# Kernel tuning notes

Measured on AMD Instinct MI355X. Metric: run time of the kernel, lower is better.

Reference implementation:

```python
import math
import jax, jax.numpy as jnp
import numpy as np

RES = [16, 32, 64, 128, 256, 512, 1024, 2048]  # base=16, finest=2048, 8 levels, growth=2
FD = 2            # feature_dim per grid level
LPE_N = 128
NF = 4            # lpe_n_freq
D0 = 8            # lpe_d0
LPE_OUT = D0 + 4 * NF  # 24
HID = 64
T = 4             # num_textures
EPS = 1e-6


def _gather_bilerp(grid, u, v, scale, imax, stride):
    """Bilinear gather from a flattened 2D grid. Returns (feat[B,C], lu[B,1], lv[B,1])."""
    fu = u * scale
    fv = v * scale
    i0 = jnp.clip(jnp.floor(fu).astype(jnp.int32), 0, imax)
    j0 = jnp.clip(jnp.floor(fv).astype(jnp.int32), 0, imax)
    lu = (fu - i0.astype(fu.dtype))[:, None]
    lv = (fv - j0.astype(fv.dtype))[:, None]
    idx00 = i0 + j0 * stride
    f00 = grid[idx00]
    f10 = grid[idx00 + 1]
    f01 = grid[idx00 + stride]
    f11 = grid[idx00 + 1 + stride]
    f0 = f00 * (1.0 - lu) + f10 * lu
    f1 = f01 * (1.0 - lu) + f11 * lu
    return f0 * (1.0 - lv) + f1 * lv, lu, lv


def setup_inputs() -> dict:
    key = jax.random.key(0)
    ks = jax.random.split(key, 24)
    B = 1048576
    inp = {"coords": jax.random.uniform(ks[0], (B, 2), jnp.float32)}
    for i, r in enumerate(RES):
        inp[f"grid{i}"] = jax.random.uniform(ks[1 + i], (r * r, FD), jnp.float32, -1e-4, 1e-4)
    inp["lpe_grid"] = jax.random.uniform(ks[9], ((LPE_N + 1) ** 2, LPE_OUT), jnp.float32, -1e-4, 1e-4)
    in_dim = FD + LPE_OUT  # 26
    inp["w0"] = jax.random.normal(ks[10], (in_dim, HID), jnp.float32) / math.sqrt(in_dim)
    inp["b0"] = jnp.zeros((HID,), jnp.float32)
    inp["w1"] = jax.random.normal(ks[11], (HID, HID), jnp.float32) / math.sqrt(HID)
    inp["b1"] = jnp.zeros((HID,), jnp.float32)
    inp["w2"] = jax.random.normal(ks[12], (HID, T), jnp.float32) / math.sqrt(HID)
    inp["b2"] = jnp.zeros((T,), jnp.float32)
    return inp


def _forward(coords, grids, lpe_grid, w0, b0, w1, b1, w2, b2):
    c = jnp.clip(coords, 0.0, 1.0 - EPS)
    u = c[:, 0]
    v = c[:, 1]
    # Multi-resolution feature grids, residual-fused (sum over levels)
    enc = jnp.zeros((coords.shape[0], FD), jnp.float32)
    for r, g in zip(RES, grids):
        f, _, _ = _gather_bilerp(g, u, v, float(r - 1), r - 2, r)
        enc = enc + f
    # Local positional encoding on (N+1)^2 grid
    coeff, lu, lv = _gather_bilerp(lpe_grid, u, v, float(LPE_N), LPE_N - 1, LPE_N + 1)
    freqs = (2.0 ** jnp.arange(NF, dtype=jnp.float32)) * (2.0 * math.pi)  # [NF]
    uu = lu * freqs[None, :]
    vv = lv * freqs[None, :]
    pe = jnp.concatenate([jnp.cos(uu), jnp.sin(uu), jnp.cos(vv), jnp.sin(vv)], axis=1)  # [B,4*NF]
    base = coeff[:, :D0]
    gate = coeff[:, D0:D0 + 4 * NF]
    lpe_out = jnp.concatenate([base, gate * pe], axis=1)  # [B,LPE_OUT]
    feat = jnp.concatenate([enc, lpe_out], axis=1)  # [B,26]
    h = jax.nn.relu(feat @ w0 + b0)
    h = jax.nn.relu(h @ w1 + b1)
    return jax.nn.sigmoid(h @ w2 + b2)  # [B,T]


def reference(coords, grid0, grid1, grid2, grid3, grid4, grid5, grid6, grid7,
              lpe_grid, w0, b0, w1, b1, w2, b2):
    grids = (grid0, grid1, grid2, grid3, grid4, grid5, grid6, grid7)
    return _forward(coords, grids, lpe_grid, w0, b0, w1, b1, w2, b2)
```

## Files before the change

### kernel.cpp

```cpp
#include <hip/hip_runtime.h>
#include <math.h>

typedef short bf16x8 __attribute__((ext_vector_type(8)));
typedef float f32x16 __attribute__((ext_vector_type(16)));
typedef float f32x4 __attribute__((ext_vector_type(4)));
typedef unsigned u32x4 __attribute__((ext_vector_type(4)));

#define NF 4
#define D0 8
#define LPE_OUT 24
#define NBUCKET 512
#define NROWS   512

#define PART_OFF   17408ULL
#define TOT_OFF    1065984ULL
#define LPE_OFF    1068544ULL
#define SCOORD_OFF 1867776ULL
#define PERM_OFF   10256384ULL
#define G6B_OFF    14450688ULL
#define G7B_OFF    18644992ULL
#define WS_NEED    35422208ULL

__device__ __forceinline__ unsigned f2bf(float x) {
    unsigned u = __float_as_uint(x);
    u = u + 0x7fffu + ((u >> 16) & 1u);
    return u >> 16;
}
__device__ __forceinline__ unsigned pkbf(float a, float b) {
    return f2bf(a) | (f2bf(b) << 16);
}
__device__ __forceinline__ float bflo(unsigned u) { return __uint_as_float(u << 16); }
__device__ __forceinline__ float bfhi(unsigned u) { return __uint_as_float(u & 0xffff0000u); }
__device__ __forceinline__ bf16x8 mkfrag(unsigned w0, unsigned w1, unsigned w2, unsigned w3) {
    u32x4 u = { w0, w1, w2, w3 };
    return __builtin_bit_cast(bf16x8, u);
}

__device__ void prep_body(const float* __restrict__ w0, const float* __restrict__ b0,
                          const float* __restrict__ w1, const float* __restrict__ b1,
                          const float* __restrict__ w2, float* __restrict__ ws, int t)
{
    unsigned short* a0 = (unsigned short*)ws;
    unsigned short* a1 = a0 + 2048;
    unsigned short* a2 = a1 + 4096;
    float* b0c = (float*)(a2 + 2048);
    float* b1c = b0c + 64;

    for (int e = t; e < 2048; e += 256) {
        int tile = e >> 9, lane = (e >> 3) & 63, j = e & 7;
        int m = tile >> 1, ks = tile & 1;
        int row = m * 32 + (lane & 31);
        int k = ks * 16 + (lane >> 5) * 8 + j;
        float v = (k < 26) ? w0[k * 64 + row] : 0.f;
        a0[e] = (unsigned short)f2bf(v);
    }
    for (int e = t; e < 4096; e += 256) {
        int tile = e >> 9, lane = (e >> 3) & 63, j = e & 7;
        int m = tile >> 2, ks = tile & 3;
        int row = m * 32 + (lane & 31);
        int k = ks * 16 + (lane >> 5) * 8 + j;
        a1[e] = (unsigned short)f2bf(w1[k * 64 + row]);
    }
    for (int e = t; e < 2048; e += 256) {
        int ks = e >> 9, lane = (e >> 3) & 63, j = e & 7;
        int row = lane & 31;
        int k = ks * 16 + (lane >> 5) * 8 + j;
        float v = (row < 4) ? w2[k * 4 + row] : 0.f;
        a2[e] = (unsigned short)f2bf(v);
    }
    if (t < 64) {
        int m = t >> 5, q5 = (t >> 4) & 1, r = t & 15;
        int row = (r & 3) + 8 * (r >> 2) + 4 * q5;
        b0c[(m * 2 + q5) * 16 + r] = b0[m * 32 + row];
        b1c[(m * 2 + q5) * 16 + r] = b1[m * 32 + row];
    }
}

__global__ void prep_kernel(const float* __restrict__ w0, const float* __restrict__ b0,
                            const float* __restrict__ w1, const float* __restrict__ b1,
                            const float* __restrict__ w2, float* __restrict__ ws)
{
    prep_body(w0, b0, w1, b1, w2, ws, threadIdx.x);
}

__device__ __forceinline__ int bucket_of(float cx, float cy) {
    float u = fminf(fmaxf(cx, 0.f), 1.f - 1e-6f);
    float v = fminf(fmaxf(cy, 0.f), 1.f - 1e-6f);
    return (int)(v * 32.f) * 16 + (int)(u * 16.f);
}

__global__ __launch_bounds__(256)
void fused_pre(const float2* __restrict__ g6, const float2* __restrict__ g7,
               const float4* __restrict__ lpe4, const float2* __restrict__ coords,
               unsigned* __restrict__ part, unsigned* __restrict__ totals,
               const float* __restrict__ w0, const float* __restrict__ b0,
               const float* __restrict__ w1, const float* __restrict__ b1,
               const float* __restrict__ w2, float* __restrict__ ws, char* __restrict__ wsb)
{
    int b = blockIdx.x, t = threadIdx.x;
    if (b < 16384) {
        int cell = b * 256 + t;
        float2 f = g7[cell];
        ((unsigned*)(wsb + G7B_OFF))[cell] = pkbf(f.x, f.y);
        return;
    }
    if (b < 20480) {
        int cell = (b - 16384) * 256 + t;
        float2 f = g6[cell];
        ((unsigned*)(wsb + G6B_OFF))[cell] = pkbf(f.x, f.y);
        return;
    }
    if (b < 20676) {
        int i = (b - 20480) * 256 + t;
        if (i < 49923) {
            float4 a = lpe4[i * 2], c = lpe4[i * 2 + 1];
            u32x4 o = { pkbf(a.x, a.y), pkbf(a.z, a.w), pkbf(c.x, c.y), pkbf(c.z, c.w) };
            ((u32x4*)(wsb + LPE_OFF))[i] = o;
        }
        return;
    }
    if (b < 21188) {
        int hb = b - 20676;
        __shared__ unsigned h[NBUCKET];
        h[t] = 0; h[t + 256] = 0;
        __syncthreads();
        for (int k = 0; k < 8; ++k) {
            float2 c = coords[hb * 2048 + k * 256 + t];
            atomicAdd(&h[bucket_of(c.x, c.y)], 1u);
        }
        __syncthreads();
        unsigned v0 = h[t], v1 = h[t + 256];
        part[hb * NBUCKET + t] = v0;
        part[hb * NBUCKET + 256 + t] = v1;
        if (v0) atomicAdd(&totals[t], v0);
        if (v1) atomicAdd(&totals[t + 256], v1);
        return;
    }
    prep_body(w0, b0, w1, b1, w2, ws, t);
}

__global__ __launch_bounds__(256)
void sort_offsets(unsigned* __restrict__ part, const unsigned* __restrict__ totals)
{
    int bucket = blockIdx.x, t = threadIdx.x;
    __shared__ unsigned red[256];
    unsigned s0 = (t < bucket) ? totals[t] : 0u;
    if (t + 256 < bucket) s0 += totals[t + 256];
    red[t] = s0;
    __syncthreads();
    for (int off = 128; off > 0; off >>= 1) {
        if (t < off) red[t] += red[t + off];
        __syncthreads();
    }
    unsigned start = red[0];
    __syncthreads();

    unsigned l0 = part[(2 * t) * NBUCKET + bucket];
    unsigned l1 = part[(2 * t + 1) * NBUCKET + bucket];
    unsigned s = l0 + l1;
    __shared__ unsigned sc[256];
    sc[t] = s;
    __syncthreads();
    for (int off = 1; off < 256; off <<= 1) {
        unsigned v = (t >= off) ? sc[t - off] : 0u;
        __syncthreads();
        sc[t] += v;
        __syncthreads();
    }
    unsigned base = start + sc[t] - s;
    part[(2 * t) * NBUCKET + bucket] = base;
    part[(2 * t + 1) * NBUCKET + bucket] = base + l0;
}

__global__ __launch_bounds__(256)
void sort_scatter(const float2* __restrict__ coords, const unsigned* __restrict__ offs,
                  float2* __restrict__ scoord, unsigned* __restrict__ perm)
{
    __shared__ unsigned cnt[NBUCKET];
    __shared__ unsigned base[NBUCKET];
    int t = threadIdx.x, hb = blockIdx.x;
    cnt[t] = 0; cnt[t + 256] = 0;
    base[t] = offs[hb * NBUCKET + t];
    base[t + 256] = offs[hb * NBUCKET + 256 + t];
    __syncthreads();
    for (int k = 0; k < 8; ++k) {
        int i = hb * 2048 + k * 256 + t;
        float2 c = coords[i];
        int bb = bucket_of(c.x, c.y);
        unsigned r = atomicAdd(&cnt[bb], 1u);
        unsigned slot = base[bb] + r;
        scoord[slot] = c;
        perm[slot] = (unsigned)i;
    }
}

__device__ __forceinline__ void mlp_pair(const unsigned (&B0)[2][2][4],
                                         const float* __restrict__ ws,
                                         const float* __restrict__ b2,
                                         int lane, int q5, f32x16 (&acc2)[2])
{
    const bf16x8* A0 = (const bf16x8*)ws;
    const bf16x8* A1 = (const bf16x8*)((const char*)ws + 4096);
    const bf16x8* A2 = (const bf16x8*)((const char*)ws + 12288);
    const float4* b0c = (const float4*)((const char*)ws + 16384);
    const float4* b1c = (const float4*)((const char*)ws + 16640);

    unsigned B1[4][2][4];
#pragma unroll
    for (int m = 0; m < 2; ++m) {
        f32x16 acc[2];
#pragma unroll
        for (int cc = 0; cc < 4; ++cc) {
            float4 bq = b0c[(m * 2 + q5) * 4 + cc];
#pragma unroll
            for (int n = 0; n < 2; ++n) {
                acc[n][4 * cc + 0] = bq.x;
                acc[n][4 * cc + 1] = bq.y;
                acc[n][4 * cc + 2] = bq.z;
                acc[n][4 * cc + 3] = bq.w;
            }
        }
#pragma unroll
        for (int ks = 0; ks < 2; ++ks) {
            bf16x8 af = A0[(m * 2 + ks) * 64 + lane];
#pragma unroll
            for (int n = 0; n < 2; ++n)
                acc[n] = __builtin_amdgcn_mfma_f32_32x32x16_bf16(
                    af, mkfrag(B0[ks][n][0], B0[ks][n][1], B0[ks][n][2], B0[ks][n][3]),
                    acc[n], 0, 0, 0);
        }
#pragma unroll
        for (int t = 0; t < 2; ++t) {
#pragma unroll
            for (int n = 0; n < 2; ++n)
#pragma unroll
                for (int c = 0; c < 2; ++c) {
                    int r0 = 2 * c + 8 * t;
                    int r1 = 2 * c + 8 * t + 4;
                    unsigned P0 = pkbf(fmaxf(acc[n][r0], 0.f), fmaxf(acc[n][r0 + 1], 0.f));
                    unsigned P1 = pkbf(fmaxf(acc[n][r1], 0.f), fmaxf(acc[n][r1 + 1], 0.f));
                    auto r = __builtin_amdgcn_permlane32_swap(P1, P0, false, false);
                    B1[2 * m + t][n][c] = r[1];
                    B1[2 * m + t][n][2 + c] = r[0];
                }
        }
    }

    unsigned B2[4][2][4];
#pragma unroll
    for (int m = 0; m < 2; ++m) {
        f32x16 acc[2];
#pragma unroll
        for (int cc = 0; cc < 4; ++cc) {
            float4 bq = b1c[(m * 2 + q5) * 4 + cc];
#pragma unroll
            for (int n = 0; n < 2; ++n) {
                acc[n][4 * cc + 0] = bq.x;
                acc[n][4 * cc + 1] = bq.y;
                acc[n][4 * cc + 2] = bq.z;
                acc[n][4 * cc + 3] = bq.w;
            }
        }
#pragma unroll
        for (int ks = 0; ks < 4; ++ks) {
            bf16x8 af = A1[(m * 4 + ks) * 64 + lane];
#pragma unroll
            for (int n = 0; n < 2; ++n)
                acc[n] = __builtin_amdgcn_mfma_f32_32x32x16_bf16(
                    af, mkfrag(B1[ks][n][0], B1[ks][n][1], B1[ks][n][2], B1[ks][n][3]),
                    acc[n], 0, 0, 0);
        }
#pragma unroll
        for (int t = 0; t < 2; ++t) {
#pragma unroll
            for (int n = 0; n < 2; ++n)
#pragma unroll
                for (int c = 0; c < 2; ++c) {
                    int r0 = 2 * c + 8 * t;
                    int r1 = 2 * c + 8 * t + 4;
                    unsigned P0 = pkbf(fmaxf(acc[n][r0], 0.f), fmaxf(acc[n][r0 + 1], 0.f));
                    unsigned P1 = pkbf(fmaxf(acc[n][r1], 0.f), fmaxf(acc[n][r1 + 1], 0.f));
                    auto r = __builtin_amdgcn_permlane32_swap(P1, P0, false, false);
                    B2[2 * m + t][n][c] = r[1];
                    B2[2 * m + t][n][2 + c] = r[0];
                }
        }
    }

#pragma unroll
    for (int n = 0; n < 2; ++n)
#pragma unroll
        for (int r = 0; r < 16; ++r) acc2[n][r] = (r < 4) ? b2[r] : 0.f;
#pragma unroll
    for (int ks = 0; ks < 4; ++ks) {
        bf16x8 af = A2[ks * 64 + lane];
#pragma unroll
        for (int n = 0; n < 2; ++n)
            acc2[n] = __builtin_amdgcn_mfma_f32_32x32x16_bf16(
                af, mkfrag(B2[ks][n][0], B2[ks][n][1], B2[ks][n][2], B2[ks][n][3]),
                acc2[n], 0, 0, 0);
    }
}

__global__ __launch_bounds__(256, 4)
void colornet_sorted(const float2* __restrict__ pts,
                     const unsigned* __restrict__ perm,
                     const float2* __restrict__ g0, const float2* __restrict__ g1,
                     const float2* __restrict__ g2, const float2* __restrict__ g3,
                     const float2* __restrict__ g4, const float2* __restrict__ g5,
                     const float* __restrict__ ws,
                     const float* __restrict__ b2,
                     f32x4* __restrict__ out)
{
    const int lane = threadIdx.x & 63;
    const int wave = threadIdx.x >> 6;
    const int q5 = lane >> 5;
    int bid = blockIdx.x;
    int cpx = gridDim.x >> 3;
    bid = (bid & 7) * cpx + (bid >> 3);
    const int base_pt = bid * 256 + wave * 64;
    const char* wsb = (const char*)ws;

    float2 c = pts[base_pt + lane];
    float uA = fminf(fmaxf(c.x, 0.f), 1.f - 1e-6f);
    float vA = fminf(fmaxf(c.y, 0.f), 1.f - 1e-6f);

    float e0A = 0.f, e1A = 0.f;

#define ADDR(IDX, R) int gx##IDX; float lu##IDX, lv##IDX; \
    { float fu_ = uA * (float)((R) - 1), fv_ = vA * (float)((R) - 1); \
      int i0_ = (int)floorf(fu_), j0_ = (int)floorf(fv_); \
      i0_ = i0_ < 0 ? 0 : (i0_ > (R) - 2 ? (R) - 2 : i0_); \
      j0_ = j0_ < 0 ? 0 : (j0_ > (R) - 2 ? (R) - 2 : j0_); \
      lu##IDX = fu_ - (float)i0_; lv##IDX = fv_ - (float)j0_; \
      gx##IDX = i0_ + j0_ * (R); }
    ADDR(7, 2048) ADDR(6, 1024) ADDR(5, 512) ADDR(4, 256)
    ADDR(3, 128)  ADDR(2, 64)   ADDR(1, 32)  ADDR(0, 16)

    const unsigned* G7 = (const unsigned*)(wsb + G7B_OFF);
    const unsigned* G6 = (const unsigned*)(wsb + G6B_OFF);
    unsigned t7_0 = G7[gx7], t7_1 = G7[gx7 + 1], t7_2 = G7[gx7 + 2048], t7_3 = G7[gx7 + 2049];
    unsigned t6_0 = G6[gx6], t6_1 = G6[gx6 + 1], t6_2 = G6[gx6 + 1024], t6_3 = G6[gx6 + 1025];

#define LOADF(IDX, R, G) \
    float2 f##IDX##_0 = (G)[gx##IDX],       f##IDX##_1 = (G)[gx##IDX + 1], \
           f##IDX##_2 = (G)[gx##IDX + (R)], f##IDX##_3 = (G)[gx##IDX + (R) + 1];
    LOADF(5, 512, g5) LOADF(4, 256, g4) LOADF(3, 128, g3)
    LOADF(2, 64,  g2) LOADF(1, 32,  g1) LOADF(0, 16,  g0)

    float lu_pe, lv_pe;
    int lc;
    {
        float fu = uA * 128.f, fv = vA * 128.f;
        int i0 = (int)floorf(fu);
        int j0 = (int)floorf(fv);
        i0 = i0 < 0 ? 0 : (i0 > 127 ? 127 : i0);
        j0 = j0 < 0 ? 0 : (j0 > 127 ? 127 : j0);
        lu_pe = fu - (float)i0;
        lv_pe = fv - (float)j0;
        lc = (i0 + j0 * 129) * 3;
    }
    const u32x4* LP = (const u32x4*)(wsb + LPE_OFF);
    u32x4 L00a = LP[lc],       L00b = LP[lc + 1],   L00c = LP[lc + 2];
    u32x4 L10a = LP[lc + 3],   L10b = LP[lc + 4],   L10c = LP[lc + 5];
    u32x4 L01a = LP[lc + 387], L01b = LP[lc + 388], L01c = LP[lc + 389];
    u32x4 L11a = LP[lc + 390], L11b = LP[lc + 391], L11c = LP[lc + 392];

    float peA[16];
#pragma unroll
    for (int kf = 0; kf < NF; ++kf) {
        float au = lu_pe * (float)(1 << kf);
        float av = lv_pe * (float)(1 << kf);
        float fu_ = __builtin_amdgcn_fractf(au);
        float fv_ = __builtin_amdgcn_fractf(av);
        peA[kf]          = __builtin_amdgcn_cosf(fu_);
        peA[NF + kf]     = __builtin_amdgcn_sinf(fu_);
        peA[2 * NF + kf] = __builtin_amdgcn_cosf(fv_);
        peA[3 * NF + kf] = __builtin_amdgcn_sinf(fv_);
    }

#define WGT(IDX) float omu##IDX = 1.f - lu##IDX, omv##IDX = 1.f - lv##IDX; \
    float w00##IDX = omu##IDX * omv##IDX, w10##IDX = lu##IDX * omv##IDX, \
          w01##IDX = omu##IDX * lv##IDX,  w11##IDX = lu##IDX * lv##IDX;
    { WGT(7)
      e0A += bflo(t7_0) * w007 + bflo(t7_1) * w107 + bflo(t7_2) * w017 + bflo(t7_3) * w117;
      e1A += bfhi(t7_0) * w007 + bfhi(t7_1) * w107 + bfhi(t7_2) * w017 + bfhi(t7_3) * w117; }
    { WGT(6)
      e0A += bflo(t6_0) * w006 + bflo(t6_1) * w106 + bflo(t6_2) * w016 + bflo(t6_3) * w116;
      e1A += bfhi(t6_0) * w006 + bfhi(t6_1) * w106 + bfhi(t6_2) * w016 + bfhi(t6_3) * w116; }
#define SUMF(IDX) { WGT(IDX) \
      e0A += f##IDX##_0.x * w00##IDX + f##IDX##_1.x * w10##IDX + f##IDX##_2.x * w01##IDX + f##IDX##_3.x * w11##IDX; \
      e1A += f##IDX##_0.y * w00##IDX + f##IDX##_1.y * w10##IDX + f##IDX##_2.y * w01##IDX + f##IDX##_3.y * w11##IDX; }
    SUMF(5) SUMF(4) SUMF(3) SUMF(2) SUMF(1) SUMF(0)

    float coeffA[LPE_OUT];
    {
        float omu = 1.f - lu_pe, omv = 1.f - lv_pe;
        float q00 = omu * omv, q10 = lu_pe * omv, q01 = omu * lv_pe, q11 = lu_pe * lv_pe;
#define LPW(W, A, B, C, Dd) \
        coeffA[2*(W)]   = bflo(A)*q00 + bflo(B)*q10 + bflo(C)*q01 + bflo(Dd)*q11; \
        coeffA[2*(W)+1] = bfhi(A)*q00 + bfhi(B)*q10 + bfhi(C)*q01 + bfhi(Dd)*q11;
        LPW(0,  L00a[0], L10a[0], L01a[0], L11a[0])
        LPW(1,  L00a[1], L10a[1], L01a[1], L11a[1])
        LPW(2,  L00a[2], L10a[2], L01a[2], L11a[2])
        LPW(3,  L00a[3], L10a[3], L01a[3], L11a[3])
        LPW(4,  L00b[0], L10b[0], L01b[0], L11b[0])
        LPW(5,  L00b[1], L10b[1], L01b[1], L11b[1])
        LPW(6,  L00b[2], L10b[2], L01b[2], L11b[2])
        LPW(7,  L00b[3], L10b[3], L01b[3], L11b[3])
        LPW(8,  L00c[0], L10c[0], L01c[0], L11c[0])
        LPW(9,  L00c[1], L10c[1], L01c[1], L11c[1])
        LPW(10, L00c[2], L10c[2], L01c[2], L11c[2])
        LPW(11, L00c[3], L10c[3], L01c[3], L11c[3])
#undef LPW
    }

    unsigned fdA[16];
    {
        float feat[32];
        feat[0] = e0A; feat[1] = e1A;
#pragma unroll
        for (int q = 0; q < D0; ++q) feat[2 + q] = coeffA[q];
#pragma unroll
        for (int q = 0; q < 4 * NF; ++q) feat[2 + D0 + q] = coeffA[D0 + q] * peA[q];
#pragma unroll
        for (int q = 26; q < 32; ++q) feat[q] = 0.f;
#pragma unroll
        for (int i = 0; i < 16; ++i) fdA[i] = pkbf(feat[2 * i], feat[2 * i + 1]);
    }

    unsigned B0a[2][2][4];
#pragma unroll
    for (int ks = 0; ks < 2; ++ks)
#pragma unroll
        for (int j2 = 0; j2 < 4; ++j2) {
            unsigned a = fdA[8 * ks + j2];
            unsigned b = fdA[8 * ks + 4 + j2];
            auto r = __builtin_amdgcn_permlane32_swap(b, a, false, false);
            B0a[ks][1][j2] = r[0];
            B0a[ks][0][j2] = r[1];
        }

    f32x16 acc2[2];
    mlp_pair(B0a, ws, b2, lane, q5, acc2);

    if (lane < 32) {
#pragma unroll
        for (int n = 0; n < 2; ++n) {
            f32x4 o;
            o[0] = 1.f / (1.f + __expf(-acc2[n][0]));
            o[1] = 1.f / (1.f + __expf(-acc2[n][1]));
            o[2] = 1.f / (1.f + __expf(-acc2[n][2]));
            o[3] = 1.f / (1.f + __expf(-acc2[n][3]));
            int oi = (int)perm[base_pt + 32 * n + lane];
            __builtin_nontemporal_store(o, out + oi);
        }
    }
}

template<int R>
__device__ __forceinline__ void gather_level(const float* __restrict__ g,
                                             float u, float v,
                                             float& e0, float& e1) {
    const float scale = (float)(R - 1);
    float fu = u * scale, fv = v * scale;
    int i0 = (int)floorf(fu);
    int j0 = (int)floorf(fv);
    i0 = i0 < 0 ? 0 : (i0 > R - 2 ? R - 2 : i0);
    j0 = j0 < 0 ? 0 : (j0 > R - 2 ? R - 2 : j0);
    float lu = fu - (float)i0;
    float lv = fv - (float)j0;
    const float2* gg = (const float2*)g;
    int base = i0 + j0 * R;
    float2 f00 = gg[base];
    float2 f10 = gg[base + 1];
    float2 f01 = gg[base + R];
    float2 f11 = gg[base + R + 1];
    float omu = 1.f - lu, omv = 1.f - lv;
    float w00 = omu * omv, w10 = lu * omv, w01 = omu * lv, w11 = lu * lv;
    e0 += f00.x * w00 + f10.x * w10 + f01.x * w01 + f11.x * w11;
    e1 += f00.y * w00 + f10.y * w10 + f01.y * w01 + f11.y * w11;
}

__global__ __launch_bounds__(256, 4)
void colornet_fp32(const float* __restrict__ coords,
                   const float* __restrict__ g0, const float* __restrict__ g1,
                   const float* __restrict__ g2, const float* __restrict__ g3,
                   const float* __restrict__ g4, const float* __restrict__ g5,
                   const float* __restrict__ g6, const float* __restrict__ g7,
                   const float* __restrict__ lpe,
                   const float* __restrict__ ws,
                   const float* __restrict__ b2,
                   f32x4* __restrict__ out)
{
    const int lane = threadIdx.x & 63;
    const int wave = threadIdx.x >> 6;
    const int q5 = lane >> 5;
    const int base_pt = blockIdx.x * 256 + wave * 64;
    const int point = base_pt + lane;

    const float* cp = coords + 2 * point;
    float cx = __builtin_nontemporal_load(cp);
    float cy = __builtin_nontemporal_load(cp + 1);
    float uA = fminf(fmaxf(cx, 0.f), 1.f - 1e-6f);
    float vA = fminf(fmaxf(cy, 0.f), 1.f - 1e-6f);

    float e0 = 0.f, e1 = 0.f;
    gather_level<16>(g0, uA, vA, e0, e1);
    gather_level<32>(g1, uA, vA, e0, e1);
    gather_level<64>(g2, uA, vA, e0, e1);
    gather_level<128>(g3, uA, vA, e0, e1);
    gather_level<256>(g4, uA, vA, e0, e1);
    gather_level<512>(g5, uA, vA, e0, e1);
    gather_level<1024>(g6, uA, vA, e0, e1);
    gather_level<2048>(g7, uA, vA, e0, e1);

    float coeff[LPE_OUT];
    float lu_pe, lv_pe;
    {
        float fu = uA * 128.f, fv = vA * 128.f;
        int i0 = (int)floorf(fu);
        int j0 = (int)floorf(fv);
        i0 = i0 < 0 ? 0 : (i0 > 127 ? 127 : i0);
        j0 = j0 < 0 ? 0 : (j0 > 127 ? 127 : j0);
        lu_pe = fu - (float)i0;
        lv_pe = fv - (float)j0;
        int base = (i0 + j0 * 129) * LPE_OUT;
        const float4* p00 = (const float4*)(lpe + base);
        const float4* p10 = (const float4*)(lpe + base + LPE_OUT);
        const float4* p01 = (const float4*)(lpe + base + 129 * LPE_OUT);
        const float4* p11 = (const float4*)(lpe + base + 130 * LPE_OUT);
        float omu = 1.f - lu_pe, omv = 1.f - lv_pe;
        float w00 = omu * omv, w10 = lu_pe * omv, w01 = omu * lv_pe, w11 = lu_pe * lv_pe;
#pragma unroll
        for (int q = 0; q < 6; ++q) {
            float4 a = p00[q], bq = p10[q], cq = p01[q], dq = p11[q];
            coeff[4 * q + 0] = a.x * w00 + bq.x * w10 + cq.x * w01 + dq.x * w11;
            coeff[4 * q + 1] = a.y * w00 + bq.y * w10 + cq.y * w01 + dq.y * w11;
            coeff[4 * q + 2] = a.z * w00 + bq.z * w10 + cq.z * w01 + dq.z * w11;
            coeff[4 * q + 3] = a.w * w00 + bq.w * w10 + cq.w * w01 + dq.w * w11;
        }
    }

    float pe[16];
#pragma unroll
    for (int kf = 0; kf < NF; ++kf) {
        const float fr = 6.28318530717958647692f * (float)(1 << kf);
        float au = lu_pe * fr;
        float av = lv_pe * fr;
        pe[kf]          = __cosf(au);
        pe[NF + kf]     = __sinf(au);
        pe[2 * NF + kf] = __cosf(av);
        pe[3 * NF + kf] = __sinf(av);
    }

    float feat[32];
    feat[0] = e0; feat[1] = e1;
#pragma unroll
    for (int q = 0; q < D0; ++q) feat[2 + q] = coeff[q];
#pragma unroll
    for (int q = 0; q < 4 * NF; ++q) feat[2 + D0 + q] = coeff[D0 + q] * pe[q];
#pragma unroll
    for (int q = 26; q < 32; ++q) feat[q] = 0.f;

    unsigned fd[16];
#pragma unroll
    for (int i = 0; i < 16; ++i) fd[i] = pkbf(feat[2 * i], feat[2 * i + 1]);

    unsigned B0[2][2][4];
#pragma unroll
    for (int ks = 0; ks < 2; ++ks)
#pragma unroll
        for (int j2 = 0; j2 < 4; ++j2) {
            unsigned a = fd[8 * ks + j2];
            unsigned b = fd[8 * ks + 4 + j2];
            auto r = __builtin_amdgcn_permlane32_swap(b, a, false, false);
            B0[ks][1][j2] = r[0];
            B0[ks][0][j2] = r[1];
        }

    f32x16 acc2[2];
    mlp_pair(B0, ws, b2, lane, q5, acc2);
    if (lane < 32) {
#pragma unroll
        for (int n = 0; n < 2; ++n) {
            f32x4 o;
            o[0] = 1.f / (1.f + __expf(-acc2[n][0]));
            o[1] = 1.f / (1.f + __expf(-acc2[n][1]));
            o[2] = 1.f / (1.f + __expf(-acc2[n][2]));
            o[3] = 1.f / (1.f + __expf(-acc2[n][3]));
            __builtin_nontemporal_store(o, out + (base_pt + 32 * n + lane));
        }
    }
}

extern "C" void kernel_launch(void* const* d_in, const int* in_sizes, int n_in,
                              void* d_out, int out_size, void* d_ws, size_t ws_size,
                              hipStream_t stream) {
    const float* coords = (const float*)d_in[0];
    const float* g0 = (const float*)d_in[1];
    const float* g1 = (const float*)d_in[2];
    const float* g2 = (const float*)d_in[3];
    const float* g3 = (const float*)d_in[4];
    const float* g4 = (const float*)d_in[5];
    const float* g5 = (const float*)d_in[6];
    const float* g6 = (const float*)d_in[7];
    const float* g7 = (const float*)d_in[8];
    const float* lpe = (const float*)d_in[9];
    const float* w0 = (const float*)d_in[10];
    const float* b0 = (const float*)d_in[11];
    const float* w1 = (const float*)d_in[12];
    const float* b1 = (const float*)d_in[13];
    const float* w2 = (const float*)d_in[14];
    const float* b2 = (const float*)d_in[15];
    f32x4* out = (f32x4*)d_out;

    int B = in_sizes[0] / 2;
    char* wsb = (char*)d_ws;

    if (ws_size >= WS_NEED && B == 1048576) {
        unsigned* part   = (unsigned*)(wsb + PART_OFF);
        unsigned* totals = (unsigned*)(wsb + TOT_OFF);
        float2*   scoord = (float2*)(wsb + SCOORD_OFF);
        unsigned* perm   = (unsigned*)(wsb + PERM_OFF);
        const float2* c2 = (const float2*)coords;

        (void)hipMemsetAsync(totals, 0, NBUCKET * sizeof(unsigned), stream);
        fused_pre<<<21189, 256, 0, stream>>>((const float2*)g6, (const float2*)g7,
                                             (const float4*)lpe, c2, part, totals,
                                             w0, b0, w1, b1, w2, (float*)d_ws, wsb);
        sort_offsets<<<NBUCKET, 256, 0, stream>>>(part, totals);
        sort_scatter<<<NROWS, 256, 0, stream>>>(c2, part, scoord, perm);

        colornet_sorted<<<4096, 256, 0, stream>>>(scoord, perm,
                                                  (const float2*)g0, (const float2*)g1,
                                                  (const float2*)g2, (const float2*)g3,
                                                  (const float2*)g4, (const float2*)g5,
                                                  (const float*)d_ws, b2, out);
    } else {
        prep_kernel<<<1, 256, 0, stream>>>(w0, b0, w1, b1, w2, (float*)d_ws);
        colornet_fp32<<<B / 256, 256, 0, stream>>>(coords, g0, g1, g2, g3, g4, g5, g6, g7,
                                                   lpe, (const float*)d_ws, b2, out);
    }
}
```

Baseline: 122.0 us.

## Read LPE grid directly in fp32 and vectorize bilinear math with float2

Removes the pre-pass that converted the LPE coefficient grid to bf16 in workspace, so the main kernel now gathers the 24 fp32 coefficients per corner straight from the input as float4 loads. This drops 196 blocks from the fused preprocessing launch. Accumulations switch to 2-wide float vectors, which can lower to packed FMA instructions, and bf16 packing now goes through the HIP intrinsic. The cost is twice the gather bytes per LPE corner in the main kernel, on a grid of about 4.8 MB that likely stays cache-resident.

```diff
diff --git a/kernel.cpp b/kernel.cpp
--- a/kernel.cpp
+++ b/kernel.cpp
@@ -1,9 +1,11 @@
 #include <hip/hip_runtime.h>
+#include <hip/hip_bf16.h>
 #include <math.h>
 
 typedef short bf16x8 __attribute__((ext_vector_type(8)));
 typedef float f32x16 __attribute__((ext_vector_type(16)));
 typedef float f32x4 __attribute__((ext_vector_type(4)));
+typedef float f32x2 __attribute__((ext_vector_type(2)));
 typedef unsigned u32x4 __attribute__((ext_vector_type(4)));
 
 #define NF 4
@@ -14,7 +16,6 @@
 
 #define PART_OFF   17408ULL
 #define TOT_OFF    1065984ULL
-#define LPE_OFF    1068544ULL
 #define SCOORD_OFF 1867776ULL
 #define PERM_OFF   10256384ULL
 #define G6B_OFF    14450688ULL
@@ -27,10 +28,16 @@
     return u >> 16;
 }
 __device__ __forceinline__ unsigned pkbf(float a, float b) {
-    return f2bf(a) | (f2bf(b) << 16);
+    __hip_bfloat16 ha = __float2bfloat16(a);
+    __hip_bfloat16 hb = __float2bfloat16(b);
+    unsigned short ua, ub;
+    __builtin_memcpy(&ua, &ha, 2);
+    __builtin_memcpy(&ub, &hb, 2);
+    return (unsigned)ua | ((unsigned)ub << 16);
 }
 __device__ __forceinline__ float bflo(unsigned u) { return __uint_as_float(u << 16); }
 __device__ __forceinline__ float bfhi(unsigned u) { return __uint_as_float(u & 0xffff0000u); }
+__device__ __forceinline__ f32x2 bf2(unsigned u) { f32x2 r = { bflo(u), bfhi(u) }; return r; }
 __device__ __forceinline__ bf16x8 mkfrag(unsigned w0, unsigned w1, unsigned w2, unsigned w3) {
     u32x4 u = { w0, w1, w2, w3 };
     return __builtin_bit_cast(bf16x8, u);
@@ -91,7 +98,7 @@
 
 __global__ __launch_bounds__(256)
 void fused_pre(const float2* __restrict__ g6, const float2* __restrict__ g7,
-               const float4* __restrict__ lpe4, const float2* __restrict__ coords,
+               const float2* __restrict__ coords,
                unsigned* __restrict__ part, unsigned* __restrict__ totals,
                const float* __restrict__ w0, const float* __restrict__ b0,
                const float* __restrict__ w1, const float* __restrict__ b1,
@@ -110,17 +117,8 @@
         ((unsigned*)(wsb + G6B_OFF))[cell] = pkbf(f.x, f.y);
         return;
     }
-    if (b < 20676) {
-        int i = (b - 20480) * 256 + t;
-        if (i < 49923) {
-            float4 a = lpe4[i * 2], c = lpe4[i * 2 + 1];
-            u32x4 o = { pkbf(a.x, a.y), pkbf(a.z, a.w), pkbf(c.x, c.y), pkbf(c.z, c.w) };
-            ((u32x4*)(wsb + LPE_OFF))[i] = o;
-        }
-        return;
-    }
-    if (b < 21188) {
-        int hb = b - 20676;
+    if (b < 20992) {
+        int hb = b - 20480;
         __shared__ unsigned h[NBUCKET];
         h[t] = 0; h[t + 256] = 0;
         __syncthreads();
@@ -305,9 +303,10 @@
 __global__ __launch_bounds__(256, 4)
 void colornet_sorted(const float2* __restrict__ pts,
                      const unsigned* __restrict__ perm,
-                     const float2* __restrict__ g0, const float2* __restrict__ g1,
-                     const float2* __restrict__ g2, const float2* __restrict__ g3,
-                     const float2* __restrict__ g4, const float2* __restrict__ g5,
+                     const f32x2* __restrict__ g0, const f32x2* __restrict__ g1,
+                     const f32x2* __restrict__ g2, const f32x2* __restrict__ g3,
+                     const f32x2* __restrict__ g4, const f32x2* __restrict__ g5,
+                     const float* __restrict__ lpe,
                      const float* __restrict__ ws,
                      const float* __restrict__ b2,
                      f32x4* __restrict__ out)
@@ -324,8 +323,6 @@
     float2 c = pts[base_pt + lane];
     float uA = fminf(fmaxf(c.x, 0.f), 1.f - 1e-6f);
     float vA = fminf(fmaxf(c.y, 0.f), 1.f - 1e-6f);
-
-    float e0A = 0.f, e1A = 0.f;
 
 #define ADDR(IDX, R) int gx##IDX; float lu##IDX, lv##IDX; \
     { float fu_ = uA * (float)((R) - 1), fv_ = vA * (float)((R) - 1); \
@@ -343,13 +340,13 @@
     unsigned t6_0 = G6[gx6], t6_1 = G6[gx6 + 1], t6_2 = G6[gx6 + 1024], t6_3 = G6[gx6 + 1025];
 
 #define LOADF(IDX, R, G) \
-    float2 f##IDX##_0 = (G)[gx##IDX],       f##IDX##_1 = (G)[gx##IDX + 1], \
-           f##IDX##_2 = (G)[gx##IDX + (R)], f##IDX##_3 = (G)[gx##IDX + (R) + 1];
+    f32x2 f##IDX##_0 = (G)[gx##IDX],       f##IDX##_1 = (G)[gx##IDX + 1], \
+          f##IDX##_2 = (G)[gx##IDX + (R)], f##IDX##_3 = (G)[gx##IDX + (R) + 1];
     LOADF(5, 512, g5) LOADF(4, 256, g4) LOADF(3, 128, g3)
     LOADF(2, 64,  g2) LOADF(1, 32,  g1) LOADF(0, 16,  g0)
 
     float lu_pe, lv_pe;
-    int lc;
+    const float4 *p00, *p10, *p01, *p11;
     {
         float fu = uA * 128.f, fv = vA * 128.f;
         int i0 = (int)floorf(fu);
@@ -358,76 +355,65 @@
         j0 = j0 < 0 ? 0 : (j0 > 127 ? 127 : j0);
         lu_pe = fu - (float)i0;
         lv_pe = fv - (float)j0;
-        lc = (i0 + j0 * 129) * 3;
-    }
-    const u32x4* LP = (const u32x4*)(wsb + LPE_OFF);
-    u32x4 L00a = LP[lc],       L00b = LP[lc + 1],   L00c = LP[lc + 2];
-    u32x4 L10a = LP[lc + 3],   L10b = LP[lc + 4],   L10c = LP[lc + 5];
-    u32x4 L01a = LP[lc + 387], L01b = LP[lc + 388], L01c = LP[lc + 389];
-    u32x4 L11a = LP[lc + 390], L11b = LP[lc + 391], L11c = LP[lc + 392];
-
-    float peA[16];
+        int base = (i0 + j0 * 129) * LPE_OUT;
+        p00 = (const float4*)(lpe + base);
+        p10 = (const float4*)(lpe + base + LPE_OUT);
+        p01 = (const float4*)(lpe + base + 129 * LPE_OUT);
+        p11 = (const float4*)(lpe + base + 130 * LPE_OUT);
+    }
+
+    float pe[16];
 #pragma unroll
     for (int kf = 0; kf < NF; ++kf) {
         float au = lu_pe * (float)(1 << kf);
         float av = lv_pe * (float)(1 << kf);
         float fu_ = __builtin_amdgcn_fractf(au);
         float fv_ = __builtin_amdgcn_fractf(av);
-        peA[kf]          = __builtin_amdgcn_cosf(fu_);
-        peA[NF + kf]     = __builtin_amdgcn_sinf(fu_);
-        peA[2 * NF + kf] = __builtin_amdgcn_cosf(fv_);
-        peA[3 * NF + kf] = __builtin_amdgcn_sinf(fv_);
-    }
-
+        pe[kf]          = __builtin_amdgcn_cosf(fu_);
+        pe[NF + kf]     = __builtin_amdgcn_sinf(fu_);
+        pe[2 * NF + kf] = __builtin_amdgcn_cosf(fv_);
+        pe[3 * NF + kf] = __builtin_amdgcn_sinf(fv_);
+    }
+
+    f32x2 eA = { 0.f, 0.f };
 #define WGT(IDX) float omu##IDX = 1.f - lu##IDX, omv##IDX = 1.f - lv##IDX; \
     float w00##IDX = omu##IDX * omv##IDX, w10##IDX = lu##IDX * omv##IDX, \
           w01##IDX = omu##IDX * lv##IDX,  w11##IDX = lu##IDX * lv##IDX;
     { WGT(7)
-      e0A += bflo(t7_0) * w007 + bflo(t7_1) * w107 + bflo(t7_2) * w017 + bflo(t7_3) * w117;
-      e1A += bfhi(t7_0) * w007 + bfhi(t7_1) * w107 + bfhi(t7_2) * w017 + bfhi(t7_3) * w117; }
+      eA += bf2(t7_0) * w007 + bf2(t7_1) * w107 + bf2(t7_2) * w017 + bf2(t7_3) * w117; }
     { WGT(6)
-      e0A += bflo(t6_0) * w006 + bflo(t6_1) * w106 + bflo(t6_2) * w016 + bflo(t6_3) * w116;
-      e1A += bfhi(t6_0) * w006 + bfhi(t6_1) * w106 + bfhi(t6_2) * w016 + bfhi(t6_3) * w116; }
+      eA += bf2(t6_0) * w006 + bf2(t6_1) * w106 + bf2(t6_2) * w016 + bf2(t6_3) * w116; }
 #define SUMF(IDX) { WGT(IDX) \
-      e0A += f##IDX##_0.x * w00##IDX + f##IDX##_1.x * w10##IDX + f##IDX##_2.x * w01##IDX + f##IDX##_3.x * w11##IDX; \
-      e1A += f##IDX##_0.y * w00##IDX + f##IDX##_1.y * w10##IDX + f##IDX##_2.y * w01##IDX + f##IDX##_3.y * w11##IDX; }
+      eA += f##IDX##_0 * w00##IDX + f##IDX##_1 * w10##IDX + f##IDX##_2 * w01##IDX + f##IDX##_3 * w11##IDX; }
     SUMF(5) SUMF(4) SUMF(3) SUMF(2) SUMF(1) SUMF(0)
 
-    float coeffA[LPE_OUT];
+    f32x2 cf[12];
     {
         float omu = 1.f - lu_pe, omv = 1.f - lv_pe;
         float q00 = omu * omv, q10 = lu_pe * omv, q01 = omu * lv_pe, q11 = lu_pe * lv_pe;
-#define LPW(W, A, B, C, Dd) \
-        coeffA[2*(W)]   = bflo(A)*q00 + bflo(B)*q10 + bflo(C)*q01 + bflo(Dd)*q11; \
-        coeffA[2*(W)+1] = bfhi(A)*q00 + bfhi(B)*q10 + bfhi(C)*q01 + bfhi(Dd)*q11;
-        LPW(0,  L00a[0], L10a[0], L01a[0], L11a[0])
-        LPW(1,  L00a[1], L10a[1], L01a[1], L11a[1])
-        LPW(2,  L00a[2], L10a[2], L01a[2], L11a[2])
-        LPW(3,  L00a[3], L10a[3], L01a[3], L11a[3])
-        LPW(4,  L00b[0], L10b[0], L01b[0], L11b[0])
-        LPW(5,  L00b[1], L10b[1], L01b[1], L11b[1])
-        LPW(6,  L00b[2], L10b[2], L01b[2], L11b[2])
-        LPW(7,  L00b[3], L10b[3], L01b[3], L11b[3])
-        LPW(8,  L00c[0], L10c[0], L01c[0], L11c[0])
-        LPW(9,  L00c[1], L10c[1], L01c[1], L11c[1])
-        LPW(10, L00c[2], L10c[2], L01c[2], L11c[2])
-        LPW(11, L00c[3], L10c[3], L01c[3], L11c[3])
-#undef LPW
+#pragma unroll
+        for (int q = 0; q < 6; ++q) {
+            float4 a = p00[q], bq = p10[q], cq = p01[q], dq = p11[q];
+            f32x2 alo = { a.x, a.y },  ahi = { a.z, a.w };
+            f32x2 blo = { bq.x, bq.y }, bhi = { bq.z, bq.w };
+            f32x2 clo = { cq.x, cq.y }, chi = { cq.z, cq.w };
+            f32x2 dlo = { dq.x, dq.y }, dhi = { dq.z, dq.w };
+            cf[2 * q]     = alo * q00 + blo * q10 + clo * q01 + dlo * q11;
+            cf[2 * q + 1] = ahi * q00 + bhi * q10 + chi * q01 + dhi * q11;
+        }
     }
 
     unsigned fdA[16];
-    {
-        float feat[32];
-        feat[0] = e0A; feat[1] = e1A;
-#pragma unroll
-        for (int q = 0; q < D0; ++q) feat[2 + q] = coeffA[q];
-#pragma unroll
-        for (int q = 0; q < 4 * NF; ++q) feat[2 + D0 + q] = coeffA[D0 + q] * peA[q];
-#pragma unroll
-        for (int q = 26; q < 32; ++q) feat[q] = 0.f;
-#pragma unroll
-        for (int i = 0; i < 16; ++i) fdA[i] = pkbf(feat[2 * i], feat[2 * i + 1]);
-    }
+    fdA[0] = pkbf(eA[0], eA[1]);
+#pragma unroll
+    for (int i = 0; i < 4; ++i) fdA[1 + i] = pkbf(cf[i][0], cf[i][1]);
+#pragma unroll
+    for (int i = 0; i < 8; ++i) {
+        f32x2 g = { pe[2 * i], pe[2 * i + 1] };
+        f32x2 m = cf[4 + i] * g;
+        fdA[5 + i] = pkbf(m[0], m[1]);
+    }
+    fdA[13] = 0u; fdA[14] = 0u; fdA[15] = 0u;
 
     unsigned B0a[2][2][4];
 #pragma unroll
@@ -626,17 +612,17 @@
         const float2* c2 = (const float2*)coords;
 
         (void)hipMemsetAsync(totals, 0, NBUCKET * sizeof(unsigned), stream);
-        fused_pre<<<21189, 256, 0, stream>>>((const float2*)g6, (const float2*)g7,
-                                             (const float4*)lpe, c2, part, totals,
+        fused_pre<<<20993, 256, 0, stream>>>((const float2*)g6, (const float2*)g7,
+                                             c2, part, totals,
                                              w0, b0, w1, b1, w2, (float*)d_ws, wsb);
         sort_offsets<<<NBUCKET, 256, 0, stream>>>(part, totals);
         sort_scatter<<<NROWS, 256, 0, stream>>>(c2, part, scoord, perm);
 
         colornet_sorted<<<4096, 256, 0, stream>>>(scoord, perm,
-                                                  (const float2*)g0, (const float2*)g1,
-                                                  (const float2*)g2, (const float2*)g3,
-                                                  (const float2*)g4, (const float2*)g5,
-                                                  (const float*)d_ws, b2, out);
+                                                  (const f32x2*)g0, (const f32x2*)g1,
+                                                  (const f32x2*)g2, (const f32x2*)g3,
+                                                  (const f32x2*)g4, (const f32x2*)g5,
+                                                  lpe, (const float*)d_ws, b2, out);
     } else {
         prep_kernel<<<1, 256, 0, stream>>>(w0, b0, w1, b1, w2, (float*)d_ws);
         colornet_fp32<<<B / 256, 256, 0, stream>>>(coords, g0, g1, g2, g3, g4, g5, g6, g7,
```

Measured after the change: 131.5 us. +7.7%, slower.
